# Kernel optimization log

Hardware: AMD Instinct MI355X
Metric: run time of the kernel (lower is better)

The kernel has to match this reference:

```python
import jax, jax.numpy as jnp
import numpy as np

TOP_K = 100
TAKE_POSITIVE_N = 1000  # >= TOP_K, so all over-threshold top-k entries survive the [:N] slice
POS_THR = 0.5
NEG_THR = 0.4
B, H, W, A, G = 4, 128, 128, 15, 32


def _make_boxes(key, shape):
    # valid yxyx boxes: (y1,x1) mins plus positive sizes
    k1, k2 = jax.random.split(key)
    mins = jax.random.uniform(k1, shape + (2,), minval=0.0, maxval=0.7)
    sizes = jax.random.uniform(k2, shape + (2,), minval=0.05, maxval=0.3)
    return jnp.concatenate([mins, mins + sizes], axis=-1)


def setup_inputs() -> dict:
    key = jax.random.key(0)
    kp, ka, kg, kc = jax.random.split(key, 4)
    return {
        'proposals': _make_boxes(kp, (B, H, W, A)),
        'anchors': _make_boxes(ka, (B, H, W, A)),   # unused by the layer's call(), kept for signature parity
        'gt_proposals': _make_boxes(kg, (G,)),
        'cls_prob': jax.random.uniform(kc, (B, H, W, A * 2)),
    }


def _iou(proposals, gt):
    # proposals [B,H,W,A,4] yxyx, gt [G,4] -> iou [B,H,W,G,A]
    p = proposals[:, :, :, None, :, :]          # [B,H,W,1,A,4]
    g = gt[:, None, :]                          # [G,1,4]
    inter_min = jnp.maximum(p[..., :2], g[..., :2])
    inter_max = jnp.minimum(p[..., 2:], g[..., 2:])
    inter_hw = jnp.maximum(inter_max - inter_min, 0.0)
    inter = inter_hw[..., 0] * inter_hw[..., 1]
    area_p = (p[..., 2] - p[..., 0]) * (p[..., 3] - p[..., 1])
    area_g = (g[..., 2] - g[..., 0]) * (g[..., 3] - g[..., 1])
    return inter / (area_p + area_g - inter)


def _yxyx_to_yxhw(b):
    y1, x1, y2, x2 = b[..., 0], b[..., 1], b[..., 2], b[..., 3]
    return jnp.stack(((y1 + y2) * 0.5, (x1 + x2) * 0.5, y2 - y1, x2 - x1), axis=-1)


def _forward(proposals, anchors, gt_proposals, cls_prob):
    iou = _iou(proposals, gt_proposals)                     # [B,H,W,G,A]
    flat = iou.reshape(-1)
    top_vals, top_idx = jax.lax.top_k(flat, TOP_K)          # global top-k over all pairs
    pos_mask = (top_vals > POS_THR).astype(iou.dtype)       # [K]; TAKE_POSITIVE_N >= K keeps all
    bi, hi, wi, gi, ai = jnp.unravel_index(top_idx, iou.shape)
    cls5 = cls_prob.reshape(B, H, W, A, 2)
    pos_props = proposals[bi, hi, wi, ai]                   # [K,4]
    pos_cls = cls5[bi, hi, wi, ai]                          # [K,2]
    pos_gt = gt_proposals[gi]                               # [K,4]
    pos_gt_cls = jnp.stack((jnp.ones(TOP_K, iou.dtype), jnp.zeros(TOP_K, iou.dtype)), axis=-1)
    n_pos = pos_mask.sum()
    # negatives: positions whose best IoU over all gt is below the negative threshold
    iou_per_position = iou.max(axis=3)                      # [B,H,W,A]
    neg_flat = (iou_per_position < NEG_THR).astype(iou.dtype).reshape(-1)
    neg_vals, neg_idx = jax.lax.top_k(neg_flat, TOP_K)      # deterministic pick of K negatives
    neg_mask = ((neg_vals > 0) & (jnp.arange(TOP_K) < n_pos)).astype(iou.dtype)
    nb, nh, nw, na = jnp.unravel_index(neg_idx, iou_per_position.shape)
    neg_cls = cls5[nb, nh, nw, na]                          # [K,2]
    neg_gt_cls = jnp.stack((jnp.zeros(TOP_K, iou.dtype), jnp.ones(TOP_K, iou.dtype)), axis=-1)
    pos_yxhw = _yxyx_to_yxhw(pos_props)
    gt_yxhw = _yxyx_to_yxhw(pos_gt)
    d_y = (gt_yxhw[:, 0] - pos_yxhw[:, 0]) / pos_yxhw[:, 2]
    d_x = (gt_yxhw[:, 1] - pos_yxhw[:, 1]) / pos_yxhw[:, 3]
    d_h = (gt_yxhw[:, 2] - pos_yxhw[:, 2]) / pos_yxhw[:, 2]
    d_w = (gt_yxhw[:, 3] - pos_yxhw[:, 3]) / pos_yxhw[:, 3]
    deltas = jnp.stack((d_y, d_x, d_h, d_w), axis=-1)       # [K,4]
    pm, nm = pos_mask[:, None], neg_mask[:, None]
    out = jnp.concatenate([
        pos_yxhw * pm, pos_cls * pm, gt_yxhw * pm, pos_gt_cls * pm,
        neg_cls * nm, neg_gt_cls * nm, deltas * pm,
    ], axis=-1)                                             # [K, 20]
    return out


def reference(proposals, anchors, gt_proposals, cls_prob):
    return _forward(proposals, anchors, gt_proposals, cls_prob)
```

## Files before the change

kernel.cpp:

```cpp
#include <hip/hip_runtime.h>
#include <stdint.h>

#define BB 4
#define HH 128
#define WW 128
#define AA 15
#define GG 32
#define NPOS (BB*HH*WW*AA)
#define NBLK1 240
#define POSB 4096
#define NCHUNK (NPOS/1024)
#define NB 256
#define NBKT 16
#define SLOTB 2048
#define TOPK 100
#define CCAP 2048

#define OFF_CHUNK 0
#define OFF_FLAG  4096
#define OFF_HISTB 987136
#define OFF_BCNT  1232896
#define OFF_CAND  1248256

__device__ __forceinline__ int fine_bin(float v) {
    int b = (int)__builtin_fmaf(v, 512.0f, -256.0f);
    b = b < 0 ? 0 : (b > NB-1 ? NB-1 : b);
    return b;
}

__global__ __launch_bounds__(1024) void k_main(const float4* __restrict__ props,
                                               const float* __restrict__ gt,
                                               uint8_t* __restrict__ ws) {
    __shared__ float s_gt[GG*4];
    __shared__ uint32_t s_hist[NB];
    __shared__ uint32_t s_bcnt[NBKT];
    __shared__ uint32_t s_red[64];
    int tid = threadIdx.x;
    if (tid < GG*4) s_gt[tid] = gt[tid];
    if (tid < NB) s_hist[tid] = 0u;
    if (tid < NBKT) s_bcnt[tid] = 0u;
    __syncthreads();

    uint2* candB = (uint2*)(ws + OFF_CAND) + (size_t)blockIdx.x * NBKT * SLOTB;

    for (int k = 0; k < 4; ++k) {
        int pos = blockIdx.x * POSB + k*1024 + tid;
        float4 p = props[pos];
        float area_p = (p.z - p.x) * (p.w - p.y);
        int bhw = pos / AA;
        int a = pos - bhw * AA;
        bool neg = true;
        #pragma unroll
        for (int g = 0; g < GG; ++g) {
            float gy1 = s_gt[g*4+0], gx1 = s_gt[g*4+1];
            float gy2 = s_gt[g*4+2], gx2 = s_gt[g*4+3];
            float ih = fmaxf(fminf(p.z, gy2) - fmaxf(p.x, gy1), 0.0f);
            float iw = fmaxf(fminf(p.w, gx2) - fmaxf(p.y, gx1), 0.0f);
            float inter = ih * iw;
            float area_g = (gy2 - gy1) * (gx2 - gx1);
            float u = area_p + area_g - inter;
            if (inter > 0.39f * u) {
                float v = inter / u;
                neg = neg && (v < 0.4f);
                if (v > 0.5f) {
                    int bin = fine_bin(v);
                    atomicAdd(&s_hist[bin], 1u);
                    int bkt = bin >> 4;
                    uint32_t slot = atomicAdd(&s_bcnt[bkt], 1u);
                    if (slot < SLOTB)
                        candB[bkt*SLOTB + slot] =
                            make_uint2(__float_as_uint(v),
                                       (uint32_t)((bhw*GG + g)*AA + a));
                }
            }
        }
        ws[OFF_FLAG + pos] = neg ? 1 : 0;
        unsigned long long bal = __ballot(neg);
        if ((tid & 63) == 0) s_red[k*16 + (tid >> 6)] = (uint32_t)__popcll(bal);
    }
    __syncthreads();
    if (tid < 4) {
        uint32_t s = 0;
        #pragma unroll
        for (int w = 0; w < 16; ++w) s += s_red[tid*16 + w];
        ((uint32_t*)(ws + OFF_CHUNK))[blockIdx.x*4 + tid] = s;
    }
    if (tid < NB) ((uint32_t*)(ws + OFF_HISTB))[blockIdx.x*NB + tid] = s_hist[tid];
    if (tid < NBKT) {
        uint32_t c = s_bcnt[tid]; if (c > SLOTB) c = SLOTB;
        ((uint32_t*)(ws + OFF_BCNT))[blockIdx.x*NBKT + tid] = c;
    }
}

__device__ __forceinline__ uint32_t incl_scan(uint32_t* s, int tid, uint32_t v) {
    s[tid] = v; __syncthreads();
    for (int st = 1; st < 1024; st <<= 1) {
        uint32_t t = (tid >= st) ? s[tid - st] : 0u;
        __syncthreads();
        s[tid] += t;
        __syncthreads();
    }
    return s[tid];
}

__global__ __launch_bounds__(1024) void k_finish(const float* __restrict__ props,
                                                 const float* __restrict__ gt,
                                                 const float* __restrict__ cls,
                                                 uint8_t* __restrict__ ws,
                                                 float* __restrict__ out) {
    __shared__ uint32_t sdata[1024];
    __shared__ uint32_t s_tot[NB];
    __shared__ float sc_v[CCAP];
    __shared__ int   sc_i[CCAP];
    __shared__ int s_posI[128];
    __shared__ int s_negI[128];
    __shared__ float s_gt[GG*4];
    __shared__ int s_T, s_M, s_c2, s_negTot;

    int tid = threadIdx.x;
    if (tid < GG*4) s_gt[tid] = gt[tid];
    if (tid == 0) { s_T = 0; s_c2 = 0; }

    {
        const uint32_t* histB = (const uint32_t*)(ws + OFF_HISTB);
        int part = tid >> 8;
        int t = tid & 255;
        uint32_t ssum = 0;
        for (int blk = part*60; blk < part*60 + 60; ++blk) ssum += histB[blk*NB + t];
        sdata[tid] = ssum;
        __syncthreads();
        if (tid < NB) s_tot[tid] = sdata[tid] + sdata[tid+256] + sdata[tid+512] + sdata[tid+768];
        __syncthreads();
    }

    if (tid < NB) sdata[tid] = s_tot[NB-1 - tid];
    __syncthreads();
    for (int st = 1; st < NB; st <<= 1) {
        uint32_t v = (tid >= st && tid < NB) ? sdata[tid - st] : 0u;
        __syncthreads();
        if (tid < NB) sdata[tid] += v;
        __syncthreads();
    }
    if (tid == 0) s_M = (int)sdata[NB-1];
    if (tid < NB) {
        uint32_t M  = sdata[NB-1];
        uint32_t ge  = sdata[NB-1 - tid];
        uint32_t geN = (tid < NB-1) ? sdata[NB-2 - tid] : 0u;
        if (M >= TOPK && ge >= TOPK && geN < TOPK) s_T = tid;
    }
    __syncthreads();
    int T = s_T;
    int M = s_M;
    int npos = M < TOPK ? M : TOPK;

    {
        const uint32_t* gbcnt = (const uint32_t*)(ws + OFF_BCNT);
        const uint2* cand0 = (const uint2*)(ws + OFF_CAND);
        int cT = T >> 4;
        int W = NBKT - cT;
        for (int pIdx = tid; pIdx < NBLK1 * W; pIdx += 1024) {
            int blk = pIdx / W;
            int bkt = cT + (pIdx - blk * W);
            uint32_t cnt = gbcnt[blk*NBKT + bkt];
            const uint2* cb = cand0 + ((size_t)blk*NBKT + bkt) * SLOTB;
            for (uint32_t j = 0; j < cnt; ++j) {
                uint2 e = cb[j];
                float v = __uint_as_float(e.x);
                if (fine_bin(v) >= T) {
                    int slot = atomicAdd(&s_c2, 1);
                    if (slot < CCAP) { sc_v[slot] = v; sc_i[slot] = (int)e.y; }
                }
            }
        }
        __syncthreads();
    }

    {
        int C2 = s_c2; if (C2 > CCAP) C2 = CCAP;
        for (int e = tid; e < C2; e += 1024) {
            float vi = sc_v[e]; int xi = sc_i[e];
            int rank = 0;
            for (int j = 0; j < C2; ++j) {
                float vj = sc_v[j]; int xj = sc_i[j];
                rank += (vj > vi) || (vj == vi && xj < xi);
            }
            if (rank < npos) s_posI[rank] = xi;
        }
        __syncthreads();
    }

    {
        const uint32_t* gchunk = (const uint32_t*)(ws + OFF_CHUNK);
        sdata[tid] = (tid < NCHUNK) ? gchunk[tid] : 0u;
        __syncthreads();
        for (int st = 512; st > 0; st >>= 1) {
            if (tid < st) sdata[tid] += sdata[tid + st];
            __syncthreads();
        }
        if (tid == 0) s_negTot = (int)sdata[0];
        __syncthreads();
    }

    {
        const uint8_t* flags = ws + OFF_FLAG;
        int base = 0;
        for (int ch = 0; ch < NCHUNK && base < TOPK; ++ch) {
            int idx = ch*1024 + tid;
            uint32_t f = flags[idx];
            uint32_t ic = incl_scan(sdata, tid, f);
            int total = (int)sdata[1023];
            if (f && (base + (int)ic - 1) < TOPK) s_negI[base + ic - 1] = idx;
            __syncthreads();
            base += total;
        }
        __syncthreads();
    }

    int i = tid;
    if (i >= TOPK) return;
    int negCount = s_negTot;
    float o[20];
    #pragma unroll
    for (int k = 0; k < 20; ++k) o[k] = 0.0f;

    if (i < npos) {
        int flat = s_posI[i];
        int a = flat % AA; int t = flat / AA;
        int g = t % GG; int bhw = t / GG;
        int pbase = (bhw * AA + a) * 4;
        float y1 = props[pbase+0], x1 = props[pbase+1];
        float y2 = props[pbase+2], x2 = props[pbase+3];
        float gy1 = s_gt[g*4+0], gx1 = s_gt[g*4+1];
        float gy2 = s_gt[g*4+2], gx2 = s_gt[g*4+3];
        float pcy = (y1 + y2) * 0.5f, pcx = (x1 + x2) * 0.5f;
        float ph = y2 - y1, pw = x2 - x1;
        float gcy = (gy1 + gy2) * 0.5f, gcx = (gx1 + gx2) * 0.5f;
        float gh = gy2 - gy1, gw = gx2 - gx1;
        int cbase = bhw * (2*AA) + 2*a;
        o[0] = pcy; o[1] = pcx; o[2] = ph; o[3] = pw;
        o[4] = cls[cbase]; o[5] = cls[cbase+1];
        o[6] = gcy; o[7] = gcx; o[8] = gh; o[9] = gw;
        o[10] = 1.0f; o[11] = 0.0f;
        if (i < negCount) {
            int nf = s_negI[i];
            int na = nf % AA; int nbhw = nf / AA;
            int nbase = nbhw * (2*AA) + 2*na;
            o[12] = cls[nbase]; o[13] = cls[nbase+1];
            o[14] = 0.0f; o[15] = 1.0f;
        }
        o[16] = (gcy - pcy) / ph;
        o[17] = (gcx - pcx) / pw;
        o[18] = (gh - ph) / ph;
        o[19] = (gw - pw) / pw;
    }
    #pragma unroll
    for (int k = 0; k < 20; ++k) out[i*20 + k] = o[k];
}

extern "C" void kernel_launch(void* const* d_in, const int* in_sizes, int n_in,
                              void* d_out, int out_size, void* d_ws, size_t ws_size,
                              hipStream_t stream) {
    (void)in_sizes; (void)n_in; (void)out_size; (void)ws_size;
    const float* props = (const float*)d_in[0];
    const float* gt = (const float*)d_in[2];
    const float* cls = (const float*)d_in[3];
    uint8_t* ws = (uint8_t*)d_ws;

    k_main<<<NBLK1, 1024, 0, stream>>>((const float4*)props, gt, ws);
    k_finish<<<1, 1024, 0, stream>>>(props, gt, cls, ws, (float*)d_out);
}
```

Baseline: 46.12 us.

## Fuse IoU pass and top-k finish into one cooperative kernel with grid sync

Merges the two kernels into one cooperative launch: all 240 blocks compute IoU histograms and candidates, then a grid-wide sync lets block 0 do the top-k selection and output. It also precomputes the gt box areas in shared memory. The aim is to remove the second kernel launch and its gap. In exchange, every block now carries the larger shared-memory footprint of the finish stage, which can lower occupancy. It also depends on all 240 blocks being co-resident, and a grid sync has its own cost.

```diff
diff --git a/kernel.cpp b/kernel.cpp
--- a/kernel.cpp
+++ b/kernel.cpp
@@ -1,5 +1,8 @@
 #include <hip/hip_runtime.h>
+#include <hip/hip_cooperative_groups.h>
 #include <stdint.h>
+
+namespace cg = cooperative_groups;
 
 #define BB 4
 #define HH 128
@@ -28,70 +31,6 @@
     return b;
 }
 
-__global__ __launch_bounds__(1024) void k_main(const float4* __restrict__ props,
-                                               const float* __restrict__ gt,
-                                               uint8_t* __restrict__ ws) {
-    __shared__ float s_gt[GG*4];
-    __shared__ uint32_t s_hist[NB];
-    __shared__ uint32_t s_bcnt[NBKT];
-    __shared__ uint32_t s_red[64];
-    int tid = threadIdx.x;
-    if (tid < GG*4) s_gt[tid] = gt[tid];
-    if (tid < NB) s_hist[tid] = 0u;
-    if (tid < NBKT) s_bcnt[tid] = 0u;
-    __syncthreads();
-
-    uint2* candB = (uint2*)(ws + OFF_CAND) + (size_t)blockIdx.x * NBKT * SLOTB;
-
-    for (int k = 0; k < 4; ++k) {
-        int pos = blockIdx.x * POSB + k*1024 + tid;
-        float4 p = props[pos];
-        float area_p = (p.z - p.x) * (p.w - p.y);
-        int bhw = pos / AA;
-        int a = pos - bhw * AA;
-        bool neg = true;
-        #pragma unroll
-        for (int g = 0; g < GG; ++g) {
-            float gy1 = s_gt[g*4+0], gx1 = s_gt[g*4+1];
-            float gy2 = s_gt[g*4+2], gx2 = s_gt[g*4+3];
-            float ih = fmaxf(fminf(p.z, gy2) - fmaxf(p.x, gy1), 0.0f);
-            float iw = fmaxf(fminf(p.w, gx2) - fmaxf(p.y, gx1), 0.0f);
-            float inter = ih * iw;
-            float area_g = (gy2 - gy1) * (gx2 - gx1);
-            float u = area_p + area_g - inter;
-            if (inter > 0.39f * u) {
-                float v = inter / u;
-                neg = neg && (v < 0.4f);
-                if (v > 0.5f) {
-                    int bin = fine_bin(v);
-                    atomicAdd(&s_hist[bin], 1u);
-                    int bkt = bin >> 4;
-                    uint32_t slot = atomicAdd(&s_bcnt[bkt], 1u);
-                    if (slot < SLOTB)
-                        candB[bkt*SLOTB + slot] =
-                            make_uint2(__float_as_uint(v),
-                                       (uint32_t)((bhw*GG + g)*AA + a));
-                }
-            }
-        }
-        ws[OFF_FLAG + pos] = neg ? 1 : 0;
-        unsigned long long bal = __ballot(neg);
-        if ((tid & 63) == 0) s_red[k*16 + (tid >> 6)] = (uint32_t)__popcll(bal);
-    }
-    __syncthreads();
-    if (tid < 4) {
-        uint32_t s = 0;
-        #pragma unroll
-        for (int w = 0; w < 16; ++w) s += s_red[tid*16 + w];
-        ((uint32_t*)(ws + OFF_CHUNK))[blockIdx.x*4 + tid] = s;
-    }
-    if (tid < NB) ((uint32_t*)(ws + OFF_HISTB))[blockIdx.x*NB + tid] = s_hist[tid];
-    if (tid < NBKT) {
-        uint32_t c = s_bcnt[tid]; if (c > SLOTB) c = SLOTB;
-        ((uint32_t*)(ws + OFF_BCNT))[blockIdx.x*NBKT + tid] = c;
-    }
-}
-
 __device__ __forceinline__ uint32_t incl_scan(uint32_t* s, int tid, uint32_t v) {
     s[tid] = v; __syncthreads();
     for (int st = 1; st < 1024; st <<= 1) {
@@ -103,22 +42,87 @@
     return s[tid];
 }
 
-__global__ __launch_bounds__(1024) void k_finish(const float* __restrict__ props,
-                                                 const float* __restrict__ gt,
-                                                 const float* __restrict__ cls,
-                                                 uint8_t* __restrict__ ws,
-                                                 float* __restrict__ out) {
+__global__ __launch_bounds__(1024, 4) void k_fused(const float4* __restrict__ props4,
+                                                   const float* __restrict__ gt,
+                                                   const float* __restrict__ cls,
+                                                   uint8_t* __restrict__ ws,
+                                                   float* __restrict__ out) {
+    __shared__ float s_gt[GG*4];
+    __shared__ float s_ga[GG];
+    __shared__ uint32_t s_hist[NB];
+    __shared__ uint32_t s_bcnt[NBKT];
+    __shared__ uint32_t s_red[64];
     __shared__ uint32_t sdata[1024];
     __shared__ uint32_t s_tot[NB];
     __shared__ float sc_v[CCAP];
     __shared__ int   sc_i[CCAP];
     __shared__ int s_posI[128];
     __shared__ int s_negI[128];
-    __shared__ float s_gt[GG*4];
     __shared__ int s_T, s_M, s_c2, s_negTot;
 
     int tid = threadIdx.x;
     if (tid < GG*4) s_gt[tid] = gt[tid];
+    if (tid < NB) s_hist[tid] = 0u;
+    if (tid < NBKT) s_bcnt[tid] = 0u;
+    __syncthreads();
+    if (tid < GG)
+        s_ga[tid] = (s_gt[tid*4+2] - s_gt[tid*4+0]) * (s_gt[tid*4+3] - s_gt[tid*4+1]);
+    __syncthreads();
+
+    {
+        uint2* candB = (uint2*)(ws + OFF_CAND) + (size_t)blockIdx.x * NBKT * SLOTB;
+        for (int k = 0; k < 4; ++k) {
+            int pos = blockIdx.x * POSB + k*1024 + tid;
+            float4 p = props4[pos];
+            float area_p = (p.z - p.x) * (p.w - p.y);
+            int bhw = pos / AA;
+            int a = pos - bhw * AA;
+            bool neg = true;
+            #pragma unroll
+            for (int g = 0; g < GG; ++g) {
+                float gy1 = s_gt[g*4+0], gx1 = s_gt[g*4+1];
+                float gy2 = s_gt[g*4+2], gx2 = s_gt[g*4+3];
+                float ih = fmaxf(fminf(p.z, gy2) - fmaxf(p.x, gy1), 0.0f);
+                float iw = fmaxf(fminf(p.w, gx2) - fmaxf(p.y, gx1), 0.0f);
+                float inter = ih * iw;
+                float u = area_p + s_ga[g] - inter;
+                if (inter > 0.39f * u) {
+                    float v = inter / u;
+                    neg = neg && (v < 0.4f);
+                    if (v > 0.5f) {
+                        int bin = fine_bin(v);
+                        atomicAdd(&s_hist[bin], 1u);
+                        int bkt = bin >> 4;
+                        uint32_t slot = atomicAdd(&s_bcnt[bkt], 1u);
+                        if (slot < SLOTB)
+                            candB[bkt*SLOTB + slot] =
+                                make_uint2(__float_as_uint(v),
+                                           (uint32_t)((bhw*GG + g)*AA + a));
+                    }
+                }
+            }
+            ws[OFF_FLAG + pos] = neg ? 1 : 0;
+            unsigned long long bal = __ballot(neg);
+            if ((tid & 63) == 0) s_red[k*16 + (tid >> 6)] = (uint32_t)__popcll(bal);
+        }
+        __syncthreads();
+        if (tid < 4) {
+            uint32_t s = 0;
+            #pragma unroll
+            for (int w = 0; w < 16; ++w) s += s_red[tid*16 + w];
+            ((uint32_t*)(ws + OFF_CHUNK))[blockIdx.x*4 + tid] = s;
+        }
+        if (tid < NB) ((uint32_t*)(ws + OFF_HISTB))[blockIdx.x*NB + tid] = s_hist[tid];
+        if (tid < NBKT) {
+            uint32_t c = s_bcnt[tid]; if (c > SLOTB) c = SLOTB;
+            ((uint32_t*)(ws + OFF_BCNT))[blockIdx.x*NBKT + tid] = c;
+        }
+    }
+
+    cg::this_grid().sync();
+    if (blockIdx.x != 0) return;
+
+    const float* props = (const float*)props4;
     if (tid == 0) { s_T = 0; s_c2 = 0; }
 
     {
@@ -143,7 +147,7 @@
     }
     if (tid == 0) s_M = (int)sdata[NB-1];
     if (tid < NB) {
-        uint32_t M  = sdata[NB-1];
+        uint32_t M   = sdata[NB-1];
         uint32_t ge  = sdata[NB-1 - tid];
         uint32_t geN = (tid < NB-1) ? sdata[NB-2 - tid] : 0u;
         if (M >= TOPK && ge >= TOPK && geN < TOPK) s_T = tid;
@@ -261,11 +265,13 @@
                               void* d_out, int out_size, void* d_ws, size_t ws_size,
                               hipStream_t stream) {
     (void)in_sizes; (void)n_in; (void)out_size; (void)ws_size;
-    const float* props = (const float*)d_in[0];
-    const float* gt = (const float*)d_in[2];
+    const float4* props4 = (const float4*)d_in[0];
+    const float* gt  = (const float*)d_in[2];
     const float* cls = (const float*)d_in[3];
     uint8_t* ws = (uint8_t*)d_ws;
-
-    k_main<<<NBLK1, 1024, 0, stream>>>((const float4*)props, gt, ws);
-    k_finish<<<1, 1024, 0, stream>>>(props, gt, cls, ws, (float*)d_out);
-}
+    float* outp = (float*)d_out;
+
+    void* args[] = { (void*)&props4, (void*)&gt, (void*)&cls, (void*)&ws, (void*)&outp };
+    hipLaunchCooperativeKernel((const void*)k_fused, dim3(NBLK1), dim3(1024),
+                               args, 0, stream);
+}
```

Result: slower. 80.20 us (+73.9%).
